# Performance work log

Hardware: AMD Instinct MI355X
Metric: run time of the kernel (lower is better)

## Reference

```python
import jax, jax.numpy as jnp
import numpy as np

B, S, D, H, P = 4, 512, 512, 8, 16
DK = D // H  # 64


def setup_inputs() -> dict:
    k0 = jax.random.key(0)
    ks = jax.random.split(k0, 10)
    std = 0.02
    lin = lambda k, shape: jax.random.normal(k, shape, dtype=jnp.float32) * std
    inp = {}
    inp["query"] = jax.random.normal(ks[0], (B, S, D), dtype=jnp.float32)
    inp["key"] = jax.random.normal(ks[1], (B, S, D), dtype=jnp.float32)
    inp["value"] = jax.random.normal(ks[2], (B, S, D), dtype=jnp.float32)
    inp["Wq"] = lin(ks[3], (D, D)); inp["bq"] = jnp.zeros((D,), jnp.float32)
    inp["Wk"] = lin(ks[4], (D, D)); inp["bk"] = jnp.zeros((D,), jnp.float32)
    inp["Wv"] = lin(ks[5], (D, D)); inp["bv"] = jnp.zeros((D,), jnp.float32)
    inp["Wo"] = lin(ks[6], (D, D)); inp["bo"] = jnp.zeros((D,), jnp.float32)
    inp["rel_table"] = lin(ks[7], (2 * P + 1, DK))  # nn.Embedding(2P+1, d_k)
    inp["gamma"] = jnp.ones((D,), jnp.float32)
    inp["beta"] = jnp.zeros((D,), jnp.float32)
    inp["mask"] = jnp.ones((B, S), dtype=jnp.int32)
    inp["relative_positions"] = jax.random.randint(ks[8], (B, S, S, DK), -32, 33, dtype=jnp.int32)
    return inp


def reference(query, key, value, Wq, bq, Wk, bk, Wv, bv, Wo, bo, rel_table, gamma, beta, mask, relative_positions):
    b, s, d = query.shape
    dk = rel_table.shape[1]
    h = d // dk
    pmax = (rel_table.shape[0] - 1) // 2

    def heads(x, W, bias):
        return (x @ W.T + bias).reshape(b, s, h, dk).transpose(0, 2, 1, 3)  # [b,h,s,dk]

    Q = heads(query, Wq, bq)
    K = heads(key, Wk, bk)
    V = heads(value, Wv, bv)

    scores = jnp.einsum('bhid,bhjd->bhij', Q, K) / jnp.sqrt(jnp.float32(dk))

    # torch: einsum('bhid,bijde->bhije', Q, emb(idx)).mean(-1)
    # mean over e commutes with the d-contraction -> pre-average the table.
    idx = jnp.clip(relative_positions, -pmax, pmax) + pmax  # [b,i,j,d]
    bias_d = rel_table.mean(axis=-1)[idx]                   # [b,i,j,d]
    scores = scores + jnp.einsum('bhid,bijd->bhij', Q, bias_d)

    scores = jnp.where(mask[:, None, None, :] == 0, jnp.float32(-1e9), scores)
    attn = jax.nn.softmax(scores, axis=-1)  # dropout is identity in eval

    ctx = jnp.einsum('bhij,bhjd->bhid', attn, V).transpose(0, 2, 1, 3).reshape(b, s, d)
    out = ctx @ Wo.T + bo

    x = out + query  # residual
    mu = x.mean(-1, keepdims=True)
    var = x.var(-1, keepdims=True)
    y = (x - mu) / jnp.sqrt(var + 1e-5) * gamma + beta
    return (y, attn)
```

## Files before the change

### kernel.cpp

```cpp
#include <hip/hip_runtime.h>
#include <hip/hip_bf16.h>

#define BB 4
#define SS 512
#define DD 512
#define HH 8
#define DK 64
#define PP 16
#define TSZ 33

typedef __bf16 bf16x8 __attribute__((ext_vector_type(8)));
typedef __bf16 bf16x4 __attribute__((ext_vector_type(4)));
typedef float  f32x4  __attribute__((ext_vector_type(4)));

union U8 { bf16x8 v; int u[4]; };

__device__ inline bf16x8 cvt8(const float* __restrict__ p) {
    f32x4 a = *(const f32x4*)p;
    f32x4 b = *(const f32x4*)(p + 4);
    bf16x8 r;
    r[0] = (__bf16)a[0]; r[1] = (__bf16)a[1]; r[2] = (__bf16)a[2]; r[3] = (__bf16)a[3];
    r[4] = (__bf16)b[0]; r[5] = (__bf16)b[1]; r[6] = (__bf16)b[2]; r[7] = (__bf16)b[3];
    return r;
}

__global__ void tmean_kernel(const float* __restrict__ rel_table, float* __restrict__ Tm) {
    int t = threadIdx.x;
    if (t < TSZ) {
        float s = 0.f;
        for (int e = 0; e < DK; ++e) s += rel_table[t * DK + e];
        Tm[t] = s * (1.f / DK);
    }
}

__global__ void proj_mfma_kernel(const float* __restrict__ X0, const float* __restrict__ X1,
                                 const float* __restrict__ X2,
                                 const float* __restrict__ W0, const float* __restrict__ W1,
                                 const float* __restrict__ W2,
                                 const float* __restrict__ B0, const float* __restrict__ B1,
                                 const float* __restrict__ B2,
                                 __bf16* __restrict__ O0, __bf16* __restrict__ O1,
                                 __bf16* __restrict__ O2) {
    int z = blockIdx.z;
    const float* X = (z == 0) ? X0 : (z == 1) ? X1 : X2;
    const float* W = (z == 0) ? W0 : (z == 1) ? W1 : W2;
    const float* bias = (z == 0) ? B0 : (z == 1) ? B1 : B2;
    __bf16* out = (z == 0) ? O0 : (z == 1) ? O1 : O2;
    int mode = (z == 2);

    int lane = threadIdx.x, wave = threadIdx.y;
    int tm = blockIdx.y * 4 + wave;
    int tn = blockIdx.x;
    int m = lane & 15, quad = lane >> 4;

    const float* arow = X + (size_t)(tm * 16 + m) * DD + quad * 8;
    const float* brow = W + (size_t)(tn * 16 + m) * DD + quad * 8;

    f32x4 acc = {0.f, 0.f, 0.f, 0.f};
    for (int k0 = 0; k0 < DD; k0 += 32) {
        bf16x8 a = cvt8(arow + k0);
        bf16x8 b = cvt8(brow + k0);
        acc = __builtin_amdgcn_mfma_f32_16x16x32_bf16(a, b, acc, 0, 0, 0);
    }

    int col = tn * 16 + m;
    int h = col >> 6, dk = col & (DK - 1);
    float bv = bias[col];
#pragma unroll
    for (int r = 0; r < 4; ++r) {
        int rowg = tm * 16 + quad * 4 + r;
        int b = rowg >> 9, i = rowg & (SS - 1);
        float v = acc[r] + bv;
        if (mode == 0)
            out[((size_t)(b * HH + h) * SS + i) * DK + dk] = (__bf16)v;
        else
            out[((size_t)(b * HH + h) * DK + dk) * SS + i] = (__bf16)v;
    }
}

__launch_bounds__(512, 2)
__global__ void f1_kernel(const __bf16* __restrict__ Qbf, const __bf16* __restrict__ Kbf,
                          const int* __restrict__ relpos, const float* __restrict__ Tm,
                          const int* __restrict__ mask, float* __restrict__ attn,
                          float* __restrict__ pm, float* __restrict__ pl) {
    __shared__ float bias_sh[8 * 16 * 132];

    int l = threadIdx.x, w = threadIdx.y;
    int jq = blockIdx.x, i0 = blockIdx.y, b = blockIdx.z;
    int m = l & 15, quad = l >> 4;

    float tmf = Tm[l < TSZ ? l : 0];
    int tmb = (int)__builtin_bit_cast(unsigned short, (__bf16)tmf);

    {
        const int ISTR = SS * DK;
        const int* rbase = relpos + ((size_t)(b * SS + i0 * 16) * SS + jq * 128 + w * 16 + m) * DK + quad * 8;
        int4 u0 = *(const int4*)(rbase);
        int4 u1 = *(const int4*)(rbase + 4);
        int4 u2 = *(const int4*)(rbase + 32);
        int4 u3 = *(const int4*)(rbase + 36);
        for (int i = 0; i < 16; ++i) {
            int4 n0, n1, n2, n3;
            if (i < 15) {
                const int* nb = rbase + (i + 1) * ISTR;
                n0 = *(const int4*)(nb);
                n1 = *(const int4*)(nb + 4);
                n2 = *(const int4*)(nb + 32);
                n3 = *(const int4*)(nb + 36);
            }
            const __bf16* qp = Qbf + ((size_t)(b * HH + (m & 7)) * SS + i0 * 16 + i) * DK + quad * 8;
            bf16x8 A0 = *(const bf16x8*)qp;
            bf16x8 A1 = *(const bf16x8*)(qp + 32);
#define LUT(vv) __builtin_amdgcn_ds_bpermute((min(max((vv), -PP), PP) + PP) << 2, tmb)
            U8 Bf0, Bf1;
            Bf0.u[0] = LUT(u0.x) | (LUT(u0.y) << 16);
            Bf0.u[1] = LUT(u0.z) | (LUT(u0.w) << 16);
            Bf0.u[2] = LUT(u1.x) | (LUT(u1.y) << 16);
            Bf0.u[3] = LUT(u1.z) | (LUT(u1.w) << 16);
            Bf1.u[0] = LUT(u2.x) | (LUT(u2.y) << 16);
            Bf1.u[1] = LUT(u2.z) | (LUT(u2.w) << 16);
            Bf1.u[2] = LUT(u3.x) | (LUT(u3.y) << 16);
            Bf1.u[3] = LUT(u3.z) | (LUT(u3.w) << 16);
#undef LUT
            f32x4 accB = {0.f, 0.f, 0.f, 0.f};
            accB = __builtin_amdgcn_mfma_f32_16x16x32_bf16(A0, Bf0.v, accB, 0, 0, 0);
            accB = __builtin_amdgcn_mfma_f32_16x16x32_bf16(A1, Bf1.v, accB, 0, 0, 0);
            if (quad < 2) {
#pragma unroll
                for (int r = 0; r < 4; ++r) {
                    int h = quad * 4 + r;
                    bias_sh[h * 2112 + i * 132 + w * 16 + m] = accB[r];
                }
            }
            u0 = n0; u1 = n1; u2 = n2; u3 = n3;
        }
    }

    const __bf16* qrow = Qbf + ((size_t)(b * HH + w) * SS + i0 * 16 + m) * DK + quad * 8;
    bf16x8 a0 = *(const bf16x8*)qrow;
    bf16x8 a1 = *(const bf16x8*)(qrow + 32);

    f32x4 acc[8];
#pragma unroll
    for (int jt = 0; jt < 8; ++jt) {
        const __bf16* krow = Kbf + ((size_t)(b * HH + w) * SS + jq * 128 + jt * 16 + m) * DK + quad * 8;
        bf16x8 b0 = *(const bf16x8*)krow;
        bf16x8 b1 = *(const bf16x8*)(krow + 32);
        f32x4 c = {0.f, 0.f, 0.f, 0.f};
        c = __builtin_amdgcn_mfma_f32_16x16x32_bf16(a0, b0, c, 0, 0, 0);
        c = __builtin_amdgcn_mfma_f32_16x16x32_bf16(a1, b1, c, 0, 0, 0);
        acc[jt] = c;
    }

    __syncthreads();

#pragma unroll
    for (int jt = 0; jt < 8; ++jt) {
#pragma unroll
        for (int r = 0; r < 4; ++r) {
            float bv = bias_sh[w * 2112 + (quad * 4 + r) * 132 + jt * 16 + m];
            acc[jt][r] = acc[jt][r] * 0.125f + bv;
        }
    }

#pragma unroll
    for (int jt = 0; jt < 8; ++jt) {
        int mv = mask[b * SS + jq * 128 + jt * 16 + m];
        if (mv == 0) {
#pragma unroll
            for (int r = 0; r < 4; ++r) acc[jt][r] = -1e9f;
        }
    }

#pragma unroll
    for (int r = 0; r < 4; ++r) {
        float mx = -1e30f;
#pragma unroll
        for (int jt = 0; jt < 8; ++jt) mx = fmaxf(mx, acc[jt][r]);
        mx = fmaxf(mx, __shfl_xor(mx, 1));
        mx = fmaxf(mx, __shfl_xor(mx, 2));
        mx = fmaxf(mx, __shfl_xor(mx, 4));
        mx = fmaxf(mx, __shfl_xor(mx, 8));
        float sum = 0.f;
#pragma unroll
        for (int jt = 0; jt < 8; ++jt) {
            float e = __expf(acc[jt][r] - mx);
            acc[jt][r] = e;
            sum += e;
        }
        sum += __shfl_xor(sum, 1);
        sum += __shfl_xor(sum, 2);
        sum += __shfl_xor(sum, 4);
        sum += __shfl_xor(sum, 8);
        if (m == 0) {
            int row = i0 * 16 + quad * 4 + r;
            pm[((size_t)(b * HH + w) * SS + row) * 4 + jq] = mx;
            pl[((size_t)(b * HH + w) * SS + row) * 4 + jq] = sum;
        }
    }

#pragma unroll
    for (int jt = 0; jt < 8; ++jt) {
#pragma unroll
        for (int r = 0; r < 4; ++r) {
            attn[((size_t)(b * HH + w) * SS + i0 * 16 + quad * 4 + r) * SS
                 + jq * 128 + jt * 16 + m] = acc[jt][r];
        }
    }
}

__launch_bounds__(256, 4)
__global__ void f2_kernel(float* __restrict__ attn, const float* __restrict__ pm,
                          const float* __restrict__ pl, const __bf16* __restrict__ Vt,
                          __bf16* __restrict__ ctx_bsd) {
    __shared__ float scl[4][16];
    __shared__ __bf16 p_sh[16 * 520];

    int t = threadIdx.x;
    int l = t & 63, wv = t >> 6;
    int i0 = blockIdx.x, bh = blockIdx.y;

    if (t < 16) {
        int row = i0 * 16 + t;
        float m0 = pm[((size_t)bh * SS + row) * 4 + 0];
        float m1 = pm[((size_t)bh * SS + row) * 4 + 1];
        float m2 = pm[((size_t)bh * SS + row) * 4 + 2];
        float m3 = pm[((size_t)bh * SS + row) * 4 + 3];
        float l0 = pl[((size_t)bh * SS + row) * 4 + 0];
        float l1 = pl[((size_t)bh * SS + row) * 4 + 1];
        float l2 = pl[((size_t)bh * SS + row) * 4 + 2];
        float l3 = pl[((size_t)bh * SS + row) * 4 + 3];
        float M = fmaxf(fmaxf(m0, m1), fmaxf(m2, m3));
        float e0 = __expf(m0 - M), e1 = __expf(m1 - M);
        float e2 = __expf(m2 - M), e3 = __expf(m3 - M);
        float L = l0 * e0 + l1 * e1 + l2 * e2 + l3 * e3;
        float inv = 1.f / L;
        scl[0][t] = e0 * inv; scl[1][t] = e1 * inv;
        scl[2][t] = e2 * inv; scl[3][t] = e3 * inv;
    }
    __syncthreads();

    float* arow = attn + ((size_t)bh * SS + i0 * 16) * SS;
#pragma unroll
    for (int rr = 0; rr < 4; ++rr) {
        int row = wv * 4 + rr;
#pragma unroll
        for (int it = 0; it < 2; ++it) {
            int col = it * 256 + l * 4;
            f32x4 v = *(f32x4*)(arow + (size_t)row * SS + col);
            float s = scl[col >> 7][row];
            v[0] *= s; v[1] *= s; v[2] *= s; v[3] *= s;
            *(f32x4*)(arow + (size_t)row * SS + col) = v;
            bf16x4 pk = {(__bf16)v[0], (__bf16)v[1], (__bf16)v[2], (__bf16)v[3]};
            *(bf16x4*)&p_sh[row * 520 + col] = pk;
        }
    }
    __syncthreads();

    int m = l & 15, quad = l >> 4;
    f32x4 acc = {0.f, 0.f, 0.f, 0.f};
    const __bf16* vrow = Vt + ((size_t)bh * DK + wv * 16 + m) * SS + quad * 8;
    for (int k0 = 0; k0 < SS; k0 += 32) {
        bf16x8 aF = *(bf16x8*)&p_sh[m * 520 + k0 + quad * 8];
        bf16x8 bF = *(const bf16x8*)(vrow + k0);
        acc = __builtin_amdgcn_mfma_f32_16x16x32_bf16(aF, bF, acc, 0, 0, 0);
    }
    int b = bh >> 3, h = bh & 7;
#pragma unroll
    for (int r = 0; r < 4; ++r) {
        ctx_bsd[((size_t)(b * SS + i0 * 16 + quad * 4 + r)) * DD + h * DK + wv * 16 + m]
            = (__bf16)acc[r];
    }
}

__global__ void outproj_mfma_kernel(const __bf16* __restrict__ Xc, const float* __restrict__ Wo,
                                    const float* __restrict__ bo, const float* __restrict__ query,
                                    float* __restrict__ xres) {
    int lane = threadIdx.x, wave = threadIdx.y;
    int tm = blockIdx.y * 4 + wave;
    int tn = blockIdx.x;
    int m = lane & 15, quad = lane >> 4;

    const __bf16* arow = Xc + (size_t)(tm * 16 + m) * DD + quad * 8;
    const float*  brow = Wo + (size_t)(tn * 16 + m) * DD + quad * 8;

    f32x4 acc = {0.f, 0.f, 0.f, 0.f};
    for (int k0 = 0; k0 < DD; k0 += 32) {
        bf16x8 a = *(const bf16x8*)(arow + k0);
        bf16x8 b = cvt8(brow + k0);
        acc = __builtin_amdgcn_mfma_f32_16x16x32_bf16(a, b, acc, 0, 0, 0);
    }

    int col = tn * 16 + m;
    float bv = bo[col];
#pragma unroll
    for (int r = 0; r < 4; ++r) {
        int rowg = tm * 16 + quad * 4 + r;
        xres[(size_t)rowg * DD + col] = acc[r] + bv + query[(size_t)rowg * DD + col];
    }
}

__global__ void ln_kernel(const float* __restrict__ x, const float* __restrict__ gamma,
                          const float* __restrict__ beta, float* __restrict__ y) {
    int r = blockIdx.x;
    int t = threadIdx.x;
    float v0 = x[r * DD + t];
    float v1 = x[r * DD + t + 256];
    __shared__ float red[4];
    float s = v0 + v1;
#pragma unroll
    for (int off = 32; off >= 1; off >>= 1) s += __shfl_xor(s, off);
    if ((t & 63) == 0) red[t >> 6] = s;
    __syncthreads();
    float mu = (red[0] + red[1] + red[2] + red[3]) * (1.f / DD);
    __syncthreads();
    float d0 = v0 - mu, d1 = v1 - mu;
    float sq = d0 * d0 + d1 * d1;
#pragma unroll
    for (int off = 32; off >= 1; off >>= 1) sq += __shfl_xor(sq, off);
    if ((t & 63) == 0) red[t >> 6] = sq;
    __syncthreads();
    float var = (red[0] + red[1] + red[2] + red[3]) * (1.f / DD);
    float inv = rsqrtf(var + 1e-5f);
    y[r * DD + t] = d0 * inv * gamma[t] + beta[t];
    y[r * DD + t + 256] = d1 * inv * gamma[t + 256] + beta[t + 256];
}

extern "C" void kernel_launch(void* const* d_in, const int* in_sizes, int n_in,
                              void* d_out, int out_size, void* d_ws, size_t ws_size,
                              hipStream_t stream) {
    const float* query  = (const float*)d_in[0];
    const float* key    = (const float*)d_in[1];
    const float* value  = (const float*)d_in[2];
    const float* Wq     = (const float*)d_in[3];
    const float* bq     = (const float*)d_in[4];
    const float* Wk     = (const float*)d_in[5];
    const float* bk     = (const float*)d_in[6];
    const float* Wv     = (const float*)d_in[7];
    const float* bv     = (const float*)d_in[8];
    const float* Wo     = (const float*)d_in[9];
    const float* bo     = (const float*)d_in[10];
    const float* rtab   = (const float*)d_in[11];
    const float* gamma  = (const float*)d_in[12];
    const float* beta   = (const float*)d_in[13];
    const int*   mask   = (const int*)d_in[14];
    const int*   relpos = (const int*)d_in[15];

    float* out = (float*)d_out;
    float* y    = out;
    float* attn = out + (size_t)BB * SS * DD;

    char* wsb = (char*)d_ws;
    float*  Tm    = (float*)wsb;   wsb += 256;
    __bf16* Qbf   = (__bf16*)wsb;  wsb += (size_t)BB * HH * SS * DK * 2;
    __bf16* Kbf   = (__bf16*)wsb;  wsb += (size_t)BB * HH * SS * DK * 2;
    __bf16* Vtbf  = (__bf16*)wsb;  wsb += (size_t)BB * HH * DK * SS * 2;
    __bf16* ctxbf = (__bf16*)wsb;  wsb += (size_t)BB * SS * DD * 2;
    float*  xres  = (float*)wsb;   wsb += (size_t)BB * SS * DD * 4;
    float*  pm    = (float*)wsb;   wsb += (size_t)BB * HH * SS * 4 * 4;
    float*  pl    = (float*)wsb;   wsb += (size_t)BB * HH * SS * 4 * 4;

    hipLaunchKernelGGL(tmean_kernel, dim3(1), dim3(64), 0, stream, rtab, Tm);

    dim3 wblk(64, 4);
    hipLaunchKernelGGL(proj_mfma_kernel, dim3(DD / 16, (BB * SS) / 64, 3), wblk, 0, stream,
                       query, key, value, Wq, Wk, Wv, bq, bk, bv, Qbf, Kbf, Vtbf);

    hipLaunchKernelGGL(f1_kernel, dim3(4, SS / 16, BB), dim3(64, 8), 0, stream,
                       Qbf, Kbf, relpos, Tm, mask, attn, pm, pl);

    hipLaunchKernelGGL(f2_kernel, dim3(SS / 16, BB * HH), dim3(256), 0, stream,
                       attn, pm, pl, Vtbf, ctxbf);

    hipLaunchKernelGGL(outproj_mfma_kernel, dim3(DD / 16, (BB * SS) / 64), wblk, 0, stream,
                       ctxbf, Wo, bo, query, xres);

    hipLaunchKernelGGL(ln_kernel, dim3(BB * SS), dim3(256), 0, stream, xres, gamma, beta, y);
}
```

Before: 541.0 us.

## Store bf16 unnormalized scores, fuse out-projection with layernorm, pre-convert Wo

f1 now writes unnormalized softmax numerators as bf16 to a workspace instead of fp32 into attn. f2 reads them, rescales, and writes the final fp32 attn with nontemporal stores. The PV matmul reads bf16 P directly from global and applies the per-chunk scale afterward, removing the fp32 read-modify-write and the LDS staging. The out-projection and layernorm are fused into one kernel using a Wo converted to bf16 in the prep kernel. f1 also gets a deeper relpos prefetch and a higher occupancy bound. The extra bf16 rounding before normalization adds some error to attn, and the variance is computed in one pass as E[x²]-mu², which is less numerically stable.

New measurement: 539.8 us. Within noise of the previous version (-0.2%).

```diff
diff --git a/kernel.cpp b/kernel.cpp
--- a/kernel.cpp
+++ b/kernel.cpp
@@ -24,12 +24,18 @@
     return r;
 }
 
-__global__ void tmean_kernel(const float* __restrict__ rel_table, float* __restrict__ Tm) {
-    int t = threadIdx.x;
-    if (t < TSZ) {
-        float s = 0.f;
-        for (int e = 0; e < DK; ++e) s += rel_table[t * DK + e];
-        Tm[t] = s * (1.f / DK);
+__global__ void prep_kernel(const float* __restrict__ rel_table, float* __restrict__ Tm,
+                            const float* __restrict__ Wo, __bf16* __restrict__ Wobf) {
+    int b = blockIdx.x, t = threadIdx.x;
+    if (b == 0) {
+        if (t < TSZ) {
+            float s = 0.f;
+            for (int e = 0; e < DK; ++e) s += rel_table[t * DK + e];
+            Tm[t] = s * (1.f / DK);
+        }
+    } else {
+        int idx = ((b - 1) * 256 + t) * 8;
+        *(bf16x8*)(Wobf + idx) = cvt8(Wo + idx);
     }
 }
 
@@ -78,10 +84,10 @@
     }
 }
 
-__launch_bounds__(512, 2)
+__launch_bounds__(512, 4)
 __global__ void f1_kernel(const __bf16* __restrict__ Qbf, const __bf16* __restrict__ Kbf,
                           const int* __restrict__ relpos, const float* __restrict__ Tm,
-                          const int* __restrict__ mask, float* __restrict__ attn,
+                          const int* __restrict__ mask, __bf16* __restrict__ pws,
                           float* __restrict__ pm, float* __restrict__ pl) {
     __shared__ float bias_sh[8 * 16 * 132];
 
@@ -99,10 +105,15 @@
         int4 u1 = *(const int4*)(rbase + 4);
         int4 u2 = *(const int4*)(rbase + 32);
         int4 u3 = *(const int4*)(rbase + 36);
+        const int* pb1 = rbase + ISTR;
+        int4 v0 = *(const int4*)(pb1);
+        int4 v1 = *(const int4*)(pb1 + 4);
+        int4 v2 = *(const int4*)(pb1 + 32);
+        int4 v3 = *(const int4*)(pb1 + 36);
         for (int i = 0; i < 16; ++i) {
             int4 n0, n1, n2, n3;
-            if (i < 15) {
-                const int* nb = rbase + (i + 1) * ISTR;
+            if (i < 14) {
+                const int* nb = rbase + (i + 2) * ISTR;
                 n0 = *(const int4*)(nb);
                 n1 = *(const int4*)(nb + 4);
                 n2 = *(const int4*)(nb + 32);
@@ -132,7 +143,8 @@
                     bias_sh[h * 2112 + i * 132 + w * 16 + m] = accB[r];
                 }
             }
-            u0 = n0; u1 = n1; u2 = n2; u3 = n3;
+            u0 = v0; u1 = v1; u2 = v2; u3 = v3;
+            v0 = n0; v1 = n1; v2 = n2; v3 = n3;
         }
     }
 
@@ -203,18 +215,17 @@
     for (int jt = 0; jt < 8; ++jt) {
 #pragma unroll
         for (int r = 0; r < 4; ++r) {
-            attn[((size_t)(b * HH + w) * SS + i0 * 16 + quad * 4 + r) * SS
-                 + jq * 128 + jt * 16 + m] = acc[jt][r];
+            pws[((size_t)(b * HH + w) * SS + i0 * 16 + quad * 4 + r) * SS
+                + jq * 128 + jt * 16 + m] = (__bf16)acc[jt][r];
         }
     }
 }
 
 __launch_bounds__(256, 4)
-__global__ void f2_kernel(float* __restrict__ attn, const float* __restrict__ pm,
+__global__ void f2_kernel(const __bf16* __restrict__ pws, const float* __restrict__ pm,
                           const float* __restrict__ pl, const __bf16* __restrict__ Vt,
-                          __bf16* __restrict__ ctx_bsd) {
+                          float* __restrict__ attn, __bf16* __restrict__ ctx_bsd) {
     __shared__ float scl[4][16];
-    __shared__ __bf16 p_sh[16 * 520];
 
     int t = threadIdx.x;
     int l = t & 63, wv = t >> 6;
@@ -222,108 +233,129 @@
 
     if (t < 16) {
         int row = i0 * 16 + t;
-        float m0 = pm[((size_t)bh * SS + row) * 4 + 0];
-        float m1 = pm[((size_t)bh * SS + row) * 4 + 1];
-        float m2 = pm[((size_t)bh * SS + row) * 4 + 2];
-        float m3 = pm[((size_t)bh * SS + row) * 4 + 3];
-        float l0 = pl[((size_t)bh * SS + row) * 4 + 0];
-        float l1 = pl[((size_t)bh * SS + row) * 4 + 1];
-        float l2 = pl[((size_t)bh * SS + row) * 4 + 2];
-        float l3 = pl[((size_t)bh * SS + row) * 4 + 3];
-        float M = fmaxf(fmaxf(m0, m1), fmaxf(m2, m3));
-        float e0 = __expf(m0 - M), e1 = __expf(m1 - M);
-        float e2 = __expf(m2 - M), e3 = __expf(m3 - M);
-        float L = l0 * e0 + l1 * e1 + l2 * e2 + l3 * e3;
+        f32x4 m4 = *(const f32x4*)(pm + ((size_t)bh * SS + row) * 4);
+        f32x4 l4 = *(const f32x4*)(pl + ((size_t)bh * SS + row) * 4);
+        float M = fmaxf(fmaxf(m4[0], m4[1]), fmaxf(m4[2], m4[3]));
+        float e0 = __expf(m4[0] - M), e1 = __expf(m4[1] - M);
+        float e2 = __expf(m4[2] - M), e3 = __expf(m4[3] - M);
+        float L = l4[0] * e0 + l4[1] * e1 + l4[2] * e2 + l4[3] * e3;
         float inv = 1.f / L;
         scl[0][t] = e0 * inv; scl[1][t] = e1 * inv;
         scl[2][t] = e2 * inv; scl[3][t] = e3 * inv;
     }
     __syncthreads();
 
-    float* arow = attn + ((size_t)bh * SS + i0 * 16) * SS;
+    const __bf16* pbase = pws + ((size_t)bh * SS + i0 * 16) * SS;
+    float* abase = attn + ((size_t)bh * SS + i0 * 16) * SS;
+
+    int colq = l >> 4;
 #pragma unroll
     for (int rr = 0; rr < 4; ++rr) {
         int row = wv * 4 + rr;
-#pragma unroll
-        for (int it = 0; it < 2; ++it) {
-            int col = it * 256 + l * 4;
-            f32x4 v = *(f32x4*)(arow + (size_t)row * SS + col);
-            float s = scl[col >> 7][row];
-            v[0] *= s; v[1] *= s; v[2] *= s; v[3] *= s;
-            *(f32x4*)(arow + (size_t)row * SS + col) = v;
-            bf16x4 pk = {(__bf16)v[0], (__bf16)v[1], (__bf16)v[2], (__bf16)v[3]};
-            *(bf16x4*)&p_sh[row * 520 + col] = pk;
-        }
-    }
-    __syncthreads();
+        bf16x8 p = *(const bf16x8*)(pbase + (size_t)row * SS + l * 8);
+        float s = scl[colq][row];
+        f32x4 o0, o1;
+        o0[0] = (float)p[0] * s; o0[1] = (float)p[1] * s;
+        o0[2] = (float)p[2] * s; o0[3] = (float)p[3] * s;
+        o1[0] = (float)p[4] * s; o1[1] = (float)p[5] * s;
+        o1[2] = (float)p[6] * s; o1[3] = (float)p[7] * s;
+        __builtin_nontemporal_store(o0, (f32x4*)(abase + (size_t)row * SS + l * 8));
+        __builtin_nontemporal_store(o1, (f32x4*)(abase + (size_t)row * SS + l * 8 + 4));
+    }
 
     int m = l & 15, quad = l >> 4;
-    f32x4 acc = {0.f, 0.f, 0.f, 0.f};
+    const __bf16* prow = pbase + (size_t)m * SS + quad * 8;
     const __bf16* vrow = Vt + ((size_t)bh * DK + wv * 16 + m) * SS + quad * 8;
-    for (int k0 = 0; k0 < SS; k0 += 32) {
-        bf16x8 aF = *(bf16x8*)&p_sh[m * 520 + k0 + quad * 8];
-        bf16x8 bF = *(const bf16x8*)(vrow + k0);
-        acc = __builtin_amdgcn_mfma_f32_16x16x32_bf16(aF, bF, acc, 0, 0, 0);
+    float ctxv[4] = {0.f, 0.f, 0.f, 0.f};
+#pragma unroll
+    for (int q = 0; q < 4; ++q) {
+        f32x4 acc = {0.f, 0.f, 0.f, 0.f};
+#pragma unroll
+        for (int kk = 0; kk < 4; ++kk) {
+            int k0 = q * 128 + kk * 32;
+            bf16x8 aF = *(const bf16x8*)(prow + k0);
+            bf16x8 bF = *(const bf16x8*)(vrow + k0);
+            acc = __builtin_amdgcn_mfma_f32_16x16x32_bf16(aF, bF, acc, 0, 0, 0);
+        }
+#pragma unroll
+        for (int r = 0; r < 4; ++r) ctxv[r] += acc[r] * scl[q][quad * 4 + r];
     }
     int b = bh >> 3, h = bh & 7;
 #pragma unroll
     for (int r = 0; r < 4; ++r) {
         ctx_bsd[((size_t)(b * SS + i0 * 16 + quad * 4 + r)) * DD + h * DK + wv * 16 + m]
-            = (__bf16)acc[r];
-    }
-}
-
-__global__ void outproj_mfma_kernel(const __bf16* __restrict__ Xc, const float* __restrict__ Wo,
-                                    const float* __restrict__ bo, const float* __restrict__ query,
-                                    float* __restrict__ xres) {
-    int lane = threadIdx.x, wave = threadIdx.y;
-    int tm = blockIdx.y * 4 + wave;
-    int tn = blockIdx.x;
+            = (__bf16)ctxv[r];
+    }
+}
+
+__launch_bounds__(512, 2)
+__global__ void outln_kernel(const __bf16* __restrict__ Xc, const __bf16* __restrict__ Wobf,
+                             const float* __restrict__ bo, const float* __restrict__ query,
+                             const float* __restrict__ gamma, const float* __restrict__ beta,
+                             float* __restrict__ y) {
+    __shared__ float xsh[16 * 516];
+
+    int lane = threadIdx.x, w = threadIdx.y;
+    int tm = blockIdx.x;
     int m = lane & 15, quad = lane >> 4;
 
     const __bf16* arow = Xc + (size_t)(tm * 16 + m) * DD + quad * 8;
-    const float*  brow = Wo + (size_t)(tn * 16 + m) * DD + quad * 8;
-
-    f32x4 acc = {0.f, 0.f, 0.f, 0.f};
+
+    f32x4 acc[4] = {{0.f,0.f,0.f,0.f},{0.f,0.f,0.f,0.f},{0.f,0.f,0.f,0.f},{0.f,0.f,0.f,0.f}};
     for (int k0 = 0; k0 < DD; k0 += 32) {
         bf16x8 a = *(const bf16x8*)(arow + k0);
-        bf16x8 b = cvt8(brow + k0);
-        acc = __builtin_amdgcn_mfma_f32_16x16x32_bf16(a, b, acc, 0, 0, 0);
-    }
-
-    int col = tn * 16 + m;
-    float bv = bo[col];
-#pragma unroll
-    for (int r = 0; r < 4; ++r) {
-        int rowg = tm * 16 + quad * 4 + r;
-        xres[(size_t)rowg * DD + col] = acc[r] + bv + query[(size_t)rowg * DD + col];
-    }
-}
-
-__global__ void ln_kernel(const float* __restrict__ x, const float* __restrict__ gamma,
-                          const float* __restrict__ beta, float* __restrict__ y) {
-    int r = blockIdx.x;
-    int t = threadIdx.x;
-    float v0 = x[r * DD + t];
-    float v1 = x[r * DD + t + 256];
-    __shared__ float red[4];
-    float s = v0 + v1;
-#pragma unroll
-    for (int off = 32; off >= 1; off >>= 1) s += __shfl_xor(s, off);
-    if ((t & 63) == 0) red[t >> 6] = s;
+#pragma unroll
+        for (int tile = 0; tile < 4; ++tile) {
+            const __bf16* brow = Wobf + (size_t)(w * 64 + tile * 16 + m) * DD + k0 + quad * 8;
+            bf16x8 b = *(const bf16x8*)brow;
+            acc[tile] = __builtin_amdgcn_mfma_f32_16x16x32_bf16(a, b, acc[tile], 0, 0, 0);
+        }
+    }
+
+#pragma unroll
+    for (int tile = 0; tile < 4; ++tile) {
+        int col = w * 64 + tile * 16 + m;
+        float bv = bo[col];
+#pragma unroll
+        for (int r = 0; r < 4; ++r) {
+            int row = quad * 4 + r;
+            int rowg = tm * 16 + row;
+            xsh[row * 516 + col] = acc[tile][r] + bv + query[(size_t)rowg * DD + col];
+        }
+    }
     __syncthreads();
-    float mu = (red[0] + red[1] + red[2] + red[3]) * (1.f / DD);
-    __syncthreads();
-    float d0 = v0 - mu, d1 = v1 - mu;
-    float sq = d0 * d0 + d1 * d1;
-#pragma unroll
-    for (int off = 32; off >= 1; off >>= 1) sq += __shfl_xor(sq, off);
-    if ((t & 63) == 0) red[t >> 6] = sq;
-    __syncthreads();
-    float var = (red[0] + red[1] + red[2] + red[3]) * (1.f / DD);
-    float inv = rsqrtf(var + 1e-5f);
-    y[r * DD + t] = d0 * inv * gamma[t] + beta[t];
-    y[r * DD + t + 256] = d1 * inv * gamma[t + 256] + beta[t + 256];
+
+#pragma unroll
+    for (int rr = 0; rr < 2; ++rr) {
+        int row = w * 2 + rr;
+        const float* xr = &xsh[row * 516];
+        f32x4 xa = *(const f32x4*)(xr + lane * 8);
+        f32x4 xb = *(const f32x4*)(xr + lane * 8 + 4);
+        float s  = xa[0] + xa[1] + xa[2] + xa[3] + xb[0] + xb[1] + xb[2] + xb[3];
+        float sq = xa[0]*xa[0] + xa[1]*xa[1] + xa[2]*xa[2] + xa[3]*xa[3]
+                 + xb[0]*xb[0] + xb[1]*xb[1] + xb[2]*xb[2] + xb[3]*xb[3];
+#pragma unroll
+        for (int off = 32; off >= 1; off >>= 1) {
+            s  += __shfl_xor(s, off);
+            sq += __shfl_xor(sq, off);
+        }
+        float mu = s * (1.f / DD);
+        float var = sq * (1.f / DD) - mu * mu;
+        float inv = rsqrtf(var + 1e-5f);
+        f32x4 g0 = *(const f32x4*)(gamma + lane * 8);
+        f32x4 g1 = *(const f32x4*)(gamma + lane * 8 + 4);
+        f32x4 b0 = *(const f32x4*)(beta + lane * 8);
+        f32x4 b1 = *(const f32x4*)(beta + lane * 8 + 4);
+        f32x4 o0, o1;
+#pragma unroll
+        for (int e = 0; e < 4; ++e) {
+            o0[e] = (xa[e] - mu) * inv * g0[e] + b0[e];
+            o1[e] = (xb[e] - mu) * inv * g1[e] + b1[e];
+        }
+        float* yr = y + (size_t)(tm * 16 + row) * DD + lane * 8;
+        *(f32x4*)yr = o0;
+        *(f32x4*)(yr + 4) = o1;
+    }
 }
 
 extern "C" void kernel_launch(void* const* d_in, const int* in_sizes, int n_in,
@@ -356,24 +388,24 @@
     __bf16* Kbf   = (__bf16*)wsb;  wsb += (size_t)BB * HH * SS * DK * 2;
     __bf16* Vtbf  = (__bf16*)wsb;  wsb += (size_t)BB * HH * DK * SS * 2;
     __bf16* ctxbf = (__bf16*)wsb;  wsb += (size_t)BB * SS * DD * 2;
-    float*  xres  = (float*)wsb;   wsb += (size_t)BB * SS * DD * 4;
+    __bf16* Wobf  = (__bf16*)wsb;  wsb += (size_t)DD * DD * 2;
+    __bf16* pws   = (__bf16*)wsb;  wsb += (size_t)BB * HH * SS * SS * 2;
     float*  pm    = (float*)wsb;   wsb += (size_t)BB * HH * SS * 4 * 4;
     float*  pl    = (float*)wsb;   wsb += (size_t)BB * HH * SS * 4 * 4;
 
-    hipLaunchKernelGGL(tmean_kernel, dim3(1), dim3(64), 0, stream, rtab, Tm);
+    hipLaunchKernelGGL(prep_kernel, dim3(1 + (DD * DD) / (256 * 8)), dim3(256), 0, stream,
+                       rtab, Tm, Wo, Wobf);
 
     dim3 wblk(64, 4);
     hipLaunchKernelGGL(proj_mfma_kernel, dim3(DD / 16, (BB * SS) / 64, 3), wblk, 0, stream,
                        query, key, value, Wq, Wk, Wv, bq, bk, bv, Qbf, Kbf, Vtbf);
 
     hipLaunchKernelGGL(f1_kernel, dim3(4, SS / 16, BB), dim3(64, 8), 0, stream,
-                       Qbf, Kbf, relpos, Tm, mask, attn, pm, pl);
+                       Qbf, Kbf, relpos, Tm, mask, pws, pm, pl);
 
     hipLaunchKernelGGL(f2_kernel, dim3(SS / 16, BB * HH), dim3(256), 0, stream,
-                       attn, pm, pl, Vtbf, ctxbf);
-
-    hipLaunchKernelGGL(outproj_mfma_kernel, dim3(DD / 16, (BB * SS) / 64), wblk, 0, stream,
-                       ctxbf, Wo, bo, query, xres);
-
-    hipLaunchKernelGGL(ln_kernel, dim3(BB * SS), dim3(256), 0, stream, xres, gamma, beta, y);
-}
+                       pws, pm, pl, Vtbf, attn, ctxbf);
+
+    hipLaunchKernelGGL(outln_kernel, dim3((BB * SS) / 16), dim3(64, 8), 0, stream,
+                       ctxbf, Wobf, bo, query, gamma, beta, y);
+}
```
